# Kernel tuning notes

Hardware: AMD Instinct MI355X
Metric: run time of the kernel (lower is better)

## Reference

```python
import jax, jax.numpy as jnp
import numpy as np

B, S, D, H = 4, 2048, 1024, 16
DH = D // H


def _rope_tables():
    # standard RoPE angle tables, shaped [1, S, 1, DH] as the module expects
    inv_freq = 1.0 / (10000.0 ** (np.arange(0, DH, 2, dtype=np.float32) / DH))
    ang = np.arange(S, dtype=np.float32)[:, None] * inv_freq[None, :]  # [S, DH/2]
    ang = np.concatenate([ang, ang], axis=-1)  # [S, DH]
    cos = jnp.asarray(np.cos(ang))[None, :, None, :]
    sin = jnp.asarray(np.sin(ang))[None, :, None, :]
    return cos, sin


def setup_inputs() -> dict:
    key = jax.random.key(0)
    ks = jax.random.split(key, 5)
    x = jax.random.normal(ks[0], (B, S, D), dtype=jnp.float32)
    wq = jax.random.normal(ks[1], (D, D), dtype=jnp.float32) * 0.02
    wk = jax.random.normal(ks[2], (D, D), dtype=jnp.float32) * 0.02
    wv = jax.random.normal(ks[3], (D, D), dtype=jnp.float32) * 0.02
    wo = jax.random.normal(ks[4], (D, D), dtype=jnp.float32) * 0.02
    cos, sin = _rope_tables()
    return {"x": x, "cos": cos, "sin": sin, "wq": wq, "wk": wk, "wv": wv, "wo": wo}


def _rotate_half(t):
    t1, t2 = t[..., : DH // 2], t[..., DH // 2:]
    return jnp.concatenate([-t2, t1], axis=-1)


def reference(x, cos, sin, wq, wk, wv, wo):
    b, s, d = x.shape
    # QKV projections (torch Linear: y = x @ W.T), reshape to [B, H, S, DH]
    q = (x @ wq.T).reshape(b, s, H, DH).transpose(0, 2, 1, 3)
    k = (x @ wk.T).reshape(b, s, H, DH).transpose(0, 2, 1, 3)
    v = (x @ wv.T).reshape(b, s, H, DH).transpose(0, 2, 1, 3)
    # permute(0,2,1,3): [1,S,1,DH] -> [1,1,S,DH]; slice [:, :s] is a no-op on the size-1 head dim
    cos_p = jnp.transpose(cos, (0, 2, 1, 3))[:, :s]
    sin_p = jnp.transpose(sin, (0, 2, 1, 3))[:, :s]
    q = q * cos_p + _rotate_half(q) * sin_p
    k = k * cos_p + _rotate_half(k) * sin_p
    # SDPA (no mask, dropout_p = 0)
    scores = jnp.einsum("bhqd,bhkd->bhqk", q, k) / jnp.sqrt(jnp.float32(DH))
    attn = jax.nn.softmax(scores, axis=-1)
    out = jnp.einsum("bhqk,bhkd->bhqd", attn, v)
    out = out.transpose(0, 2, 1, 3).reshape(b, s, d)
    return out @ wo.T
```

## Files before the change

kernel.cpp:

```cpp
#include <hip/hip_runtime.h>
#include <hip/hip_bf16.h>
#include <stdint.h>

#define B 4
#define S 2048
#define D 1024
#define H 16
#define DH 64
#define M_TOT (B*S)
#define BH (B*H)

typedef unsigned short u16;
typedef unsigned int u32;
typedef __attribute__((ext_vector_type(4))) float f32x4;
typedef __attribute__((ext_vector_type(16))) float f32x16;
typedef __attribute__((ext_vector_type(8))) short bf16x8;
typedef __attribute__((ext_vector_type(2))) unsigned int u32x2;

typedef const __attribute__((address_space(1))) unsigned int* gp_t;
typedef __attribute__((address_space(3))) unsigned int* lp_t;

__device__ __forceinline__ void gload_lds16(const void* g, void* l) {
    __builtin_amdgcn_global_load_lds((gp_t)g, (lp_t)l, 16, 0, 0);
}

__device__ __forceinline__ float bf2f(u16 u) {
    u32 t = ((u32)u) << 16;
    float f; __builtin_memcpy(&f, &t, 4); return f;
}
__device__ __forceinline__ u16 f2bf(float f) {
    u32 u; __builtin_memcpy(&u, &f, 4);
    u += 0x7fffu + ((u >> 16) & 1u);
    return (u16)(u >> 16);
}
__device__ __forceinline__ u32 packbf(float lo, float hi_) {
    __hip_bfloat162 h = __float22bfloat162_rn(float2{lo, hi_});
    u32 r; __builtin_memcpy(&r, &h, 4); return r;
}

__device__ __forceinline__ float exp2_fast(float x) { return __builtin_amdgcn_exp2f(x); }

#if __has_builtin(__builtin_amdgcn_permlane32_swap)
__device__ __forceinline__ void plswap(u32& a, u32& bb) {
    u32x2 r = __builtin_amdgcn_permlane32_swap(a, bb, false, false);
    a = r.x; bb = r.y;
}
#else
__device__ __forceinline__ void plswap(u32& a, u32& bb) {
    int hi = (threadIdx.x >> 5) & 1;
    u32 ra = (u32)__shfl_xor((int)a, 32);
    u32 rb = (u32)__shfl_xor((int)bb, 32);
    u32 na = hi ? rb : a;
    u32 nb = hi ? bb : ra;
    a = na; bb = nb;
}
#endif

__global__ __launch_bounds__(256)
void cvt_all_kernel(const float* __restrict__ x,
                    const float* __restrict__ wq, const float* __restrict__ wk,
                    const float* __restrict__ wv, const float* __restrict__ wo,
                    u16* __restrict__ xb, u16* __restrict__ wqb, u16* __restrict__ wkb,
                    u16* __restrict__ wvb, u16* __restrict__ wob)
{
    const size_t MD = (size_t)M_TOT * D;
    const size_t WD = (size_t)D * D;
    size_t i = ((size_t)blockIdx.x * 256 + threadIdx.x) * 8;
    const float* src; u16* dst; size_t off;
    if (i < MD) { src = x; dst = xb; off = i; }
    else {
        size_t j = i - MD;
        int wsel = (int)(j >> 20);
        off = j & (WD - 1);
        if      (wsel == 0) { src = wq; dst = wqb; }
        else if (wsel == 1) { src = wk; dst = wkb; }
        else if (wsel == 2) { src = wv; dst = wvb; }
        else                { src = wo; dst = wob; }
    }
    float4 a = *(const float4*)(src + off);
    float4 b = *(const float4*)(src + off + 4);
    union { u16 u[8]; bf16x8 v; } o;
    o.u[0] = f2bf(a.x); o.u[1] = f2bf(a.y); o.u[2] = f2bf(a.z); o.u[3] = f2bf(a.w);
    o.u[4] = f2bf(b.x); o.u[5] = f2bf(b.y); o.u[6] = f2bf(b.z); o.u[7] = f2bf(b.w);
    *(bf16x8*)(dst + off) = o.v;
}

#define NKT 32

__global__ __launch_bounds__(512)
void gemm256_qkv(const u16* __restrict__ X,
                 const u16* __restrict__ W0, const u16* __restrict__ W1, const u16* __restrict__ W2,
                 u16* __restrict__ Y0, u16* __restrict__ Y1, u16* __restrict__ Y2,
                 const float* __restrict__ cosT, const float* __restrict__ sinT)
{
    __shared__ __align__(16) u16 lds[65536];

    const u16* Wm = (blockIdx.z == 0) ? W0 : (blockIdx.z == 1) ? W1 : W2;
    u16* Y        = (blockIdx.z == 0) ? Y0 : (blockIdx.z == 1) ? Y1 : Y2;

    const int t  = threadIdx.x;
    const int w  = t >> 6, ll = t & 63;
    const int lc = ll & 15, g = ll >> 4;
    const int wr = w >> 2, wc = w & 3;
    const int m0 = blockIdx.x * 256, n0 = blockIdx.y * 256;

    const int srow   = t >> 2;
    const int scolsw = 8 * ((t & 3) ^ ((t >> 3) & 3));

    const u16* Xa = X + (size_t)m0 * D;
    const u16* Wa = Wm + (size_t)n0 * D;

    int offA[8], offB[4];
    #pragma unroll
    for (int i = 0; i < 8; ++i) {
        int row = wr * 128 + i * 16 + lc;
        offA[i] = row * 32 + ((g ^ ((row >> 1) & 3)) << 3);
    }
    #pragma unroll
    for (int j = 0; j < 4; ++j) {
        int row = wc * 64 + j * 16 + lc;
        offB[j] = row * 32 + ((g ^ ((row >> 1) & 3)) << 3);
    }

    f32x4 acc[8][4];
    #pragma unroll
    for (int i = 0; i < 8; ++i)
        #pragma unroll
        for (int j = 0; j < 4; ++j)
            acc[i][j] = (f32x4){0.f, 0.f, 0.f, 0.f};

    #pragma unroll
    for (int kt = 0; kt < 3; ++kt) {
        const u16* xs = Xa + (size_t)srow * D + kt * 32 + scolsw;
        gload_lds16(xs,           &lds[kt * 16384 + w * 512]);
        gload_lds16(xs + 128 * D, &lds[kt * 16384 + 4096 + w * 512]);
        const u16* ws = Wa + (size_t)srow * D + kt * 32 + scolsw;
        gload_lds16(ws,           &lds[kt * 16384 + 8192 + w * 512]);
        gload_lds16(ws + 128 * D, &lds[kt * 16384 + 8192 + 4096 + w * 512]);
    }
    asm volatile("s_waitcnt vmcnt(8)" ::: "memory");
    __builtin_amdgcn_s_barrier();

    auto body = [&](int kt, bool do_stage) {
        const int s = kt & 3;
        const u16* As = &lds[s * 16384];
        const u16* Bs = &lds[s * 16384 + 8192];
        const int kn = kt + 3;
        const int sn = kn & 3;
        if (do_stage) {
            const u16* xs = Xa + (size_t)srow * D + kn * 32 + scolsw;
            gload_lds16(xs,           &lds[sn * 16384 + w * 512]);
            gload_lds16(xs + 128 * D, &lds[sn * 16384 + 4096 + w * 512]);
        }
        bf16x8 bfr[4];
        #pragma unroll
        for (int j = 0; j < 4; ++j)
            bfr[j] = *(const bf16x8*)&Bs[offB[j]];
        bf16x8 afr[4];
        #pragma unroll
        for (int i = 0; i < 4; ++i)
            afr[i] = *(const bf16x8*)&As[offA[i]];
        #pragma unroll
        for (int i = 0; i < 4; ++i)
            #pragma unroll
            for (int j = 0; j < 4; ++j)
                acc[i][j] = __builtin_amdgcn_mfma_f32_16x16x32_bf16(afr[i], bfr[j], acc[i][j], 0, 0, 0);
        if (do_stage) {
            const u16* ws = Wa + (size_t)srow * D + kn * 32 + scolsw;
            gload_lds16(ws,           &lds[sn * 16384 + 8192 + w * 512]);
            gload_lds16(ws + 128 * D, &lds[sn * 16384 + 8192 + 4096 + w * 512]);
        }
        #pragma unroll
        for (int i = 0; i < 4; ++i)
            afr[i] = *(const bf16x8*)&As[offA[i + 4]];
        #pragma unroll
        for (int i = 0; i < 4; ++i)
            #pragma unroll
            for (int j = 0; j < 4; ++j)
                acc[i + 4][j] = __builtin_amdgcn_mfma_f32_16x16x32_bf16(afr[i], bfr[j], acc[i + 4][j], 0, 0, 0);
    };

    for (int kt = 0; kt < NKT - 3; ++kt) {
        body(kt, true);
        asm volatile("s_waitcnt vmcnt(8)" ::: "memory");
        __builtin_amdgcn_s_barrier();
    }
    body(NKT - 3, false);
    asm volatile("s_waitcnt vmcnt(4)" ::: "memory");
    __builtin_amdgcn_s_barrier();
    body(NKT - 2, false);
    asm volatile("s_waitcnt vmcnt(0)" ::: "memory");
    __builtin_amdgcn_s_barrier();
    body(NKT - 1, false);

    if (blockIdx.z < 2) {
        const float scale = (blockIdx.z == 0) ? (0.125f * 1.44269504f) : 1.0f;
        #pragma unroll
        for (int i = 0; i < 8; ++i)
            #pragma unroll
            for (int r = 0; r < 4; ++r) {
                int row = m0 + wr * 128 + i * 16 + g * 4 + r;
                int s = row & (S - 1);
                #pragma unroll
                for (int jh = 0; jh < 2; ++jh) {
                    float c  = cosT[s * DH + jh * 16 + lc];
                    float sn = sinT[s * DH + jh * 16 + lc];
                    float a0 = acc[i][jh][r], a1 = acc[i][jh + 2][r];
                    size_t base = (size_t)row * D + n0 + wc * 64;
                    Y[base + jh * 16 + lc]       = f2bf((a0 * c - a1 * sn) * scale);
                    Y[base + (jh + 2) * 16 + lc] = f2bf((a1 * c + a0 * sn) * scale);
                }
            }
    } else {
        #pragma unroll
        for (int i = 0; i < 8; ++i)
            #pragma unroll
            for (int j = 0; j < 4; ++j) {
                int row = m0 + wr * 128 + i * 16 + g * 4;
                int col = n0 + wc * 64 + j * 16 + lc;
                int bt = row >> 11, s = row & (S - 1);
                size_t vtrow = (size_t)(bt * 16 + (col >> 6)) * 64 + (col & 63);
                u32 w0 = packbf(acc[i][j][0], acc[i][j][1]);
                u32 w1 = packbf(acc[i][j][2], acc[i][j][3]);
                u32x2 pr; pr.x = w0; pr.y = w1;
                *(u32x2*)&Y[vtrow * S + s] = pr;
            }
    }
}

__global__ __launch_bounds__(256)
void gemm128_wo(const u16* __restrict__ X, const u16* __restrict__ Wm,
                float* __restrict__ Y)
{
    __shared__ __align__(16) u16 lds[32768];

    const int t  = threadIdx.x;
    const int w  = t >> 6, ll = t & 63;
    const int lc = ll & 15, g = ll >> 4;
    const int wr = w >> 1, wc = w & 1;
    const int m0 = blockIdx.x * 128, n0 = blockIdx.y * 128;

    const int srow   = t >> 2;
    const int scolsw = 8 * ((t & 3) ^ ((t >> 3) & 3));

    const u16* Xa = X + (size_t)m0 * D;
    const u16* Wa = Wm + (size_t)n0 * D;

    int offA[4], offB[4];
    #pragma unroll
    for (int i = 0; i < 4; ++i) {
        int row = wr * 64 + i * 16 + lc;
        offA[i] = row * 32 + ((g ^ ((row >> 1) & 3)) << 3);
    }
    #pragma unroll
    for (int j = 0; j < 4; ++j) {
        int row = wc * 64 + j * 16 + lc;
        offB[j] = row * 32 + ((g ^ ((row >> 1) & 3)) << 3);
    }

    f32x4 acc[4][4];
    #pragma unroll
    for (int i = 0; i < 4; ++i)
        #pragma unroll
        for (int j = 0; j < 4; ++j)
            acc[i][j] = (f32x4){0.f, 0.f, 0.f, 0.f};

    #pragma unroll
    for (int kt = 0; kt < 3; ++kt) {
        const u16* xs = Xa + (size_t)srow * D + kt * 32 + scolsw;
        gload_lds16(xs,          &lds[kt * 8192 + w * 512]);
        gload_lds16(xs + 64 * D, &lds[kt * 8192 + 2048 + w * 512]);
        const u16* ws = Wa + (size_t)srow * D + kt * 32 + scolsw;
        gload_lds16(ws,          &lds[kt * 8192 + 4096 + w * 512]);
        gload_lds16(ws + 64 * D, &lds[kt * 8192 + 4096 + 2048 + w * 512]);
    }
    asm volatile("s_waitcnt vmcnt(8)" ::: "memory");
    __builtin_amdgcn_s_barrier();

    auto body = [&](int kt, bool do_stage) {
        const int s = kt & 3;
        const u16* As = &lds[s * 8192];
        const u16* Bs = &lds[s * 8192 + 4096];
        const int kn = kt + 3;
        const int sn = kn & 3;
        if (do_stage) {
            const u16* xs = Xa + (size_t)srow * D + kn * 32 + scolsw;
            gload_lds16(xs,          &lds[sn * 8192 + w * 512]);
            gload_lds16(xs + 64 * D, &lds[sn * 8192 + 2048 + w * 512]);
        }
        bf16x8 bfr[4];
        #pragma unroll
        for (int j = 0; j < 4; ++j)
            bfr[j] = *(const bf16x8*)&Bs[offB[j]];
        bf16x8 afr[2];
        afr[0] = *(const bf16x8*)&As[offA[0]];
        afr[1] = *(const bf16x8*)&As[offA[1]];
        #pragma unroll
        for (int i = 0; i < 2; ++i)
            #pragma unroll
            for (int j = 0; j < 4; ++j)
                acc[i][j] = __builtin_amdgcn_mfma_f32_16x16x32_bf16(afr[i], bfr[j], acc[i][j], 0, 0, 0);
        if (do_stage) {
            const u16* ws = Wa + (size_t)srow * D + kn * 32 + scolsw;
            gload_lds16(ws,          &lds[sn * 8192 + 4096 + w * 512]);
            gload_lds16(ws + 64 * D, &lds[sn * 8192 + 4096 + 2048 + w * 512]);
        }
        afr[0] = *(const bf16x8*)&As[offA[2]];
        afr[1] = *(const bf16x8*)&As[offA[3]];
        #pragma unroll
        for (int i = 0; i < 2; ++i)
            #pragma unroll
            for (int j = 0; j < 4; ++j)
                acc[i + 2][j] = __builtin_amdgcn_mfma_f32_16x16x32_bf16(afr[i], bfr[j], acc[i + 2][j], 0, 0, 0);
    };

    for (int kt = 0; kt < NKT - 3; ++kt) {
        body(kt, true);
        asm volatile("s_waitcnt vmcnt(8)" ::: "memory");
        __builtin_amdgcn_s_barrier();
    }
    body(NKT - 3, false);
    asm volatile("s_waitcnt vmcnt(4)" ::: "memory");
    __builtin_amdgcn_s_barrier();
    body(NKT - 2, false);
    asm volatile("s_waitcnt vmcnt(0)" ::: "memory");
    __builtin_amdgcn_s_barrier();
    body(NKT - 1, false);

    #pragma unroll
    for (int i = 0; i < 4; ++i)
        #pragma unroll
        for (int j = 0; j < 4; ++j)
            #pragma unroll
            for (int r = 0; r < 4; ++r) {
                int row = m0 + wr * 64 + i * 16 + g * 4 + r;
                int col = n0 + wc * 64 + j * 16 + lc;
                Y[(size_t)row * D + col] = acc[i][j][r];
            }
}

#define QBLK 256
#define KVT 128
#define NT (S / KVT)

__global__ __launch_bounds__(256, 2)
void attn_mfma(const u16* __restrict__ Q, const u16* __restrict__ Kg,
               const u16* __restrict__ Vt, u16* __restrict__ CTX)
{
    __shared__ __align__(16) u16 smem[32768];

    const int t  = threadIdx.x;
    const int w  = t >> 6;
    const int q  = t & 31;
    const int hi = (t >> 5) & 1;

    const int bid  = blockIdx.x;
    const int xcd  = bid & 7;
    const int slot = bid >> 3;
    const int bh   = xcd * 8 + (slot >> 3);
    const int qb   = slot & 7;
    const int b = bh >> 4, h = bh & 15;
    const int q0 = qb * QBLK;
    const int qbase = q0 + w * 64;

    bf16x8 qf[2][4];
    #pragma unroll
    for (int qg = 0; qg < 2; ++qg) {
        const u16* qp = &Q[(size_t)(b*S + qbase + qg*32 + q) * D + h*DH + hi*8];
        qf[qg][0] = *(const bf16x8*)(qp);
        qf[qg][1] = *(const bf16x8*)(qp + 16);
        qf[qg][2] = *(const bf16x8*)(qp + 32);
        qf[qg][3] = *(const bf16x8*)(qp + 48);
    }

    bf16x8 ones;
    {
        union { u16 u[8]; bf16x8 v; } ou;
        #pragma unroll
        for (int i = 0; i < 8; ++i) ou.u[i] = 0x3f80;
        ones = ou.v;
    }

    f32x16 po[4], lsum[2], zv;
    #pragma unroll
    for (int i = 0; i < 16; ++i) {
        po[0][i] = 0.f; po[1][i] = 0.f; po[2][i] = 0.f; po[3][i] = 0.f;
        lsum[0][i] = 0.f; lsum[1][i] = 0.f; zv[i] = 0.f;
    }

    const int ksrow = t >> 3;
    const int kscol = (((t & 7) << 4) ^ ((ksrow & 7) << 4)) >> 1;
    const int vsrow = t >> 4;
    const int vscol = (((t & 15) ^ (vsrow & 15)) << 3);
    const int rsw  = (q & 7) << 4;
    const int vsw  = (q & 15) << 4;

    u16* buf0 = smem;
    u16* buf1 = smem + 16384;

    const u16* kg = Kg + ((size_t)(b * S) + ksrow) * D + (size_t)h * DH + kscol;
    const u16* vg = Vt + ((size_t)bh * DH + vsrow) * S + vscol;

    #define STAGE(dst) do {                                         \
        gload_lds16(kg,           (dst) + 0*2048 + w*512);          \
        gload_lds16(kg + 32*D,    (dst) + 1*2048 + w*512);          \
        gload_lds16(kg + 64*D,    (dst) + 2*2048 + w*512);          \
        gload_lds16(kg + 96*D,    (dst) + 3*2048 + w*512);          \
        gload_lds16(vg,           (dst) + 8192 + 0*2048 + w*512);   \
        gload_lds16(vg + 16*S,    (dst) + 8192 + 1*2048 + w*512);   \
        gload_lds16(vg + 32*S,    (dst) + 8192 + 2*2048 + w*512);   \
        gload_lds16(vg + 48*S,    (dst) + 8192 + 3*2048 + w*512);   \
        kg += (size_t)KVT * D; vg += KVT; } while (0)

    auto compute = [&](const u16* base) {
        const u16* Kl = base;
        const u16* Vl = base + 8192;
        #pragma unroll
        for (int c = 0; c < 4; ++c) {
            f32x16 p0, p1;
            {
                const u16* kr = &Kl[(c*32 + q) << 6];
                bf16x8 k0 = *(const bf16x8*)&kr[((0*32 + hi*16) ^ rsw) >> 1];
                __builtin_amdgcn_s_setprio(1);
                p0 = __builtin_amdgcn_mfma_f32_32x32x16_bf16(k0, qf[0][0], zv, 0, 0, 0);
                p1 = __builtin_amdgcn_mfma_f32_32x32x16_bf16(k0, qf[1][0], zv, 0, 0, 0);
                #pragma unroll
                for (int cc = 1; cc < 4; ++cc) {
                    bf16x8 kf = *(const bf16x8*)&kr[((cc*32 + hi*16) ^ rsw) >> 1];
                    p0 = __builtin_amdgcn_mfma_f32_32x32x16_bf16(kf, qf[0][cc], p0, 0, 0, 0);
                    p1 = __builtin_amdgcn_mfma_f32_32x32x16_bf16(kf, qf[1][cc], p1, 0, 0, 0);
                }
                __builtin_amdgcn_s_setprio(0);
            }

            u32 W0[8], W1[8];
            #pragma unroll
            for (int j = 0; j < 8; ++j) {
                W0[j] = packbf(exp2_fast(p0[2*j]), exp2_fast(p0[2*j + 1]));
                W1[j] = packbf(exp2_fast(p1[2*j]), exp2_fast(p1[2*j + 1]));
            }
            plswap(W0[0], W0[2]); plswap(W0[1], W0[3]);
            plswap(W0[4], W0[6]); plswap(W0[5], W0[7]);
            plswap(W1[0], W1[2]); plswap(W1[1], W1[3]);
            plswap(W1[4], W1[6]); plswap(W1[5], W1[7]);
            bf16x8 pa0a, pa0b, pa1a, pa1b;
            {
                union { u32 u[4]; bf16x8 v; } pb;
                pb.u[0]=W0[0]; pb.u[1]=W0[1]; pb.u[2]=W0[2]; pb.u[3]=W0[3]; pa0a = pb.v;
                pb.u[0]=W0[4]; pb.u[1]=W0[5]; pb.u[2]=W0[6]; pb.u[3]=W0[7]; pa0b = pb.v;
                pb.u[0]=W1[0]; pb.u[1]=W1[1]; pb.u[2]=W1[2]; pb.u[3]=W1[3]; pa1a = pb.v;
                pb.u[0]=W1[4]; pb.u[1]=W1[5]; pb.u[2]=W1[6]; pb.u[3]=W1[7]; pa1b = pb.v;
            }

            __builtin_amdgcn_s_setprio(1);
            lsum[0] = __builtin_amdgcn_mfma_f32_32x32x16_bf16(ones, pa0a, lsum[0], 0, 0, 0);
            lsum[1] = __builtin_amdgcn_mfma_f32_32x32x16_bf16(ones, pa1a, lsum[1], 0, 0, 0);
            lsum[0] = __builtin_amdgcn_mfma_f32_32x32x16_bf16(ones, pa0b, lsum[0], 0, 0, 0);
            lsum[1] = __builtin_amdgcn_mfma_f32_32x32x16_bf16(ones, pa1b, lsum[1], 0, 0, 0);
            #pragma unroll
            for (int kk = 0; kk < 2; ++kk) {
                int vb = ((c*64 + kk*32 + hi*16) ^ vsw) >> 1;
                bf16x8 v0 = *(const bf16x8*)&Vl[(q << 7) + vb];
                bf16x8 v1 = *(const bf16x8*)&Vl[((32 + q) << 7) + vb];
                bf16x8 pq0 = kk ? pa0b : pa0a;
                bf16x8 pq1 = kk ? pa1b : pa1a;
                po[0] = __builtin_amdgcn_mfma_f32_32x32x16_bf16(v0, pq0, po[0], 0, 0, 0);
                po[1] = __builtin_amdgcn_mfma_f32_32x32x16_bf16(v1, pq0, po[1], 0, 0, 0);
                po[2] = __builtin_amdgcn_mfma_f32_32x32x16_bf16(v0, pq1, po[2], 0, 0, 0);
                po[3] = __builtin_amdgcn_mfma_f32_32x32x16_bf16(v1, pq1, po[3], 0, 0, 0);
            }
            __builtin_amdgcn_s_setprio(0);
        }
    };

    STAGE(buf0);
    asm volatile("s_waitcnt vmcnt(0)" ::: "memory");
    __builtin_amdgcn_s_barrier();

    for (int ti = 0; ti < NT; ti += 2) {
        STAGE(buf1);
        compute(buf0);
        asm volatile("s_waitcnt vmcnt(0)" ::: "memory");
        __builtin_amdgcn_s_barrier();
        if (ti < NT - 2) STAGE(buf0);
        compute(buf1);
        asm volatile("s_waitcnt vmcnt(0)" ::: "memory");
        __builtin_amdgcn_s_barrier();
    }
    #undef STAGE

    u16* ow = &smem[w * 2304];
    #pragma unroll
    for (int qg = 0; qg < 2; ++qg) {
        float inv = 1.f / lsum[qg][0];
        #pragma unroll
        for (int r = 0; r < 16; ++r) {
            int d0 = (r & 3) + 8 * (r >> 2) + 4 * hi;
            ow[q * 72 + d0]      = f2bf(po[qg*2 + 0][r] * inv);
            ow[q * 72 + 32 + d0] = f2bf(po[qg*2 + 1][r] * inv);
        }
        int row = (t & 63) >> 1, half = t & 1;
        const u16* orow = &ow[row * 72 + half * 32];
        u16* gp = &CTX[(size_t)(b*S + qbase + qg*32 + row) * D + h*DH + half * 32];
        #pragma unroll
        for (int i = 0; i < 4; ++i)
            *(bf16x8*)(gp + i * 8) = *(const bf16x8*)(orow + i * 8);
    }
}

extern "C" void kernel_launch(void* const* d_in, const int* in_sizes, int n_in,
                              void* d_out, int out_size, void* d_ws, size_t ws_size,
                              hipStream_t stream)
{
    const float* x    = (const float*)d_in[0];
    const float* cosT = (const float*)d_in[1];
    const float* sinT = (const float*)d_in[2];
    const float* wq   = (const float*)d_in[3];
    const float* wk   = (const float*)d_in[4];
    const float* wv   = (const float*)d_in[5];
    const float* wo   = (const float*)d_in[6];
    float* out = (float*)d_out;

    const size_t MD = (size_t)M_TOT * D;
    const size_t WD = (size_t)D * D;

    u16* xb   = (u16*)d_ws;
    u16* Qb   = xb + MD;
    u16* Kb   = Qb + MD;
    u16* Vtb  = Kb + MD;
    u16* CTXb = Vtb + MD;
    u16* wqb  = CTXb + MD;
    u16* wkb  = wqb + WD;
    u16* wvb  = wkb + WD;
    u16* wob  = wvb + WD;

    cvt_all_kernel<<<(int)((MD + 4*WD) / 8 / 256), 256, 0, stream>>>(
        x, wq, wk, wv, wo, xb, wqb, wkb, wvb, wob);

    gemm256_qkv<<<dim3(M_TOT / 256, D / 256, 3), 512, 0, stream>>>(
        xb, wqb, wkb, wvb, Qb, Kb, Vtb, cosT, sinT);

    attn_mfma<<<dim3(M_TOT / QBLK * H), 256, 0, stream>>>(Qb, Kb, Vtb, CTXb);

    gemm128_wo<<<dim3(M_TOT / 128, D / 128), 256, 0, stream>>>(
        CTXb, wob, out);
}
```

Measured before the change: 177.4 us.

## Use four-stage KV pipeline with 64-key tiles in attention kernel

Replaces the double-buffered 128-key K/V staging in the attention kernel with a four-slot ring of 64-key tiles that prefetches three tiles ahead. Waits use partial vmcnt so loads stay in flight across iterations instead of draining to zero each step. The V tile layout and swizzle change to match the 64-wide rows. This adds more barriers per key and smaller tiles, which may raise synchronisation overhead.

```diff
diff --git a/kernel.cpp b/kernel.cpp
--- a/kernel.cpp
+++ b/kernel.cpp
@@ -340,8 +340,8 @@
 }
 
 #define QBLK 256
-#define KVT 128
-#define NT (S / KVT)
+#define KVT2 64
+#define NTT (S / KVT2)
 
 __global__ __launch_bounds__(256, 2)
 void attn_mfma(const u16* __restrict__ Q, const u16* __restrict__ Kg,
@@ -388,35 +388,27 @@
         lsum[0][i] = 0.f; lsum[1][i] = 0.f; zv[i] = 0.f;
     }
 
-    const int ksrow = t >> 3;
-    const int kscol = (((t & 7) << 4) ^ ((ksrow & 7) << 4)) >> 1;
-    const int vsrow = t >> 4;
-    const int vscol = (((t & 15) ^ (vsrow & 15)) << 3);
+    const int srow = t >> 3;
+    const int scol = ((t & 7) ^ ((t >> 3) & 7)) << 3;
     const int rsw  = (q & 7) << 4;
-    const int vsw  = (q & 15) << 4;
-
-    u16* buf0 = smem;
-    u16* buf1 = smem + 16384;
-
-    const u16* kg = Kg + ((size_t)(b * S) + ksrow) * D + (size_t)h * DH + kscol;
-    const u16* vg = Vt + ((size_t)bh * DH + vsrow) * S + vscol;
-
-    #define STAGE(dst) do {                                         \
-        gload_lds16(kg,           (dst) + 0*2048 + w*512);          \
-        gload_lds16(kg + 32*D,    (dst) + 1*2048 + w*512);          \
-        gload_lds16(kg + 64*D,    (dst) + 2*2048 + w*512);          \
-        gload_lds16(kg + 96*D,    (dst) + 3*2048 + w*512);          \
-        gload_lds16(vg,           (dst) + 8192 + 0*2048 + w*512);   \
-        gload_lds16(vg + 16*S,    (dst) + 8192 + 1*2048 + w*512);   \
-        gload_lds16(vg + 32*S,    (dst) + 8192 + 2*2048 + w*512);   \
-        gload_lds16(vg + 48*S,    (dst) + 8192 + 3*2048 + w*512);   \
-        kg += (size_t)KVT * D; vg += KVT; } while (0)
-
-    auto compute = [&](const u16* base) {
-        const u16* Kl = base;
-        const u16* Vl = base + 8192;
-        #pragma unroll
-        for (int c = 0; c < 4; ++c) {
+
+    const u16* kg = Kg + ((size_t)(b * S) + srow) * D + (size_t)h * DH + scol;
+    const u16* vg = Vt + ((size_t)bh * DH + srow) * S + scol;
+
+    #define STAGE(sl) do {                                       \
+        gload_lds16(kg,          &smem[(sl)*8192 + w*512]);          \
+        gload_lds16(kg + 32*D,   &smem[(sl)*8192 + 2048 + w*512]);   \
+        gload_lds16(vg,          &smem[(sl)*8192 + 4096 + w*512]);   \
+        gload_lds16(vg + 32*S,   &smem[(sl)*8192 + 4096 + 2048 + w*512]); \
+        kg += (size_t)KVT2 * D; vg += KVT2; } while (0)
+
+    auto body = [&](int kt, bool do_stage) {
+        const int sl = kt & 3;
+        const u16* Kl = &smem[sl * 8192];
+        const u16* Vl = &smem[sl * 8192 + 4096];
+        if (do_stage) { const int sn = (kt + 3) & 3; STAGE(sn); }
+        #pragma unroll
+        for (int c = 0; c < 2; ++c) {
             f32x16 p0, p1;
             {
                 const u16* kr = &Kl[(c*32 + q) << 6];
@@ -459,9 +451,9 @@
             lsum[1] = __builtin_amdgcn_mfma_f32_32x32x16_bf16(ones, pa1b, lsum[1], 0, 0, 0);
             #pragma unroll
             for (int kk = 0; kk < 2; ++kk) {
-                int vb = ((c*64 + kk*32 + hi*16) ^ vsw) >> 1;
-                bf16x8 v0 = *(const bf16x8*)&Vl[(q << 7) + vb];
-                bf16x8 v1 = *(const bf16x8*)&Vl[((32 + q) << 7) + vb];
+                int vb = ((c*64 + kk*32 + hi*16) ^ rsw) >> 1;
+                bf16x8 v0 = *(const bf16x8*)&Vl[(q << 6) + vb];
+                bf16x8 v1 = *(const bf16x8*)&Vl[((32 + q) << 6) + vb];
                 bf16x8 pq0 = kk ? pa0b : pa0a;
                 bf16x8 pq1 = kk ? pa1b : pa1a;
                 po[0] = __builtin_amdgcn_mfma_f32_32x32x16_bf16(v0, pq0, po[0], 0, 0, 0);
@@ -473,20 +465,22 @@
         }
     };
 
-    STAGE(buf0);
+    STAGE(0); STAGE(1); STAGE(2);
+    asm volatile("s_waitcnt vmcnt(8)" ::: "memory");
+    __builtin_amdgcn_s_barrier();
+
+    for (int kt = 0; kt < NTT - 3; ++kt) {
+        body(kt, true);
+        asm volatile("s_waitcnt vmcnt(8)" ::: "memory");
+        __builtin_amdgcn_s_barrier();
+    }
+    body(NTT - 3, false);
+    asm volatile("s_waitcnt vmcnt(4)" ::: "memory");
+    __builtin_amdgcn_s_barrier();
+    body(NTT - 2, false);
     asm volatile("s_waitcnt vmcnt(0)" ::: "memory");
     __builtin_amdgcn_s_barrier();
-
-    for (int ti = 0; ti < NT; ti += 2) {
-        STAGE(buf1);
-        compute(buf0);
-        asm volatile("s_waitcnt vmcnt(0)" ::: "memory");
-        __builtin_amdgcn_s_barrier();
-        if (ti < NT - 2) STAGE(buf0);
-        compute(buf1);
-        asm volatile("s_waitcnt vmcnt(0)" ::: "memory");
-        __builtin_amdgcn_s_barrier();
-    }
+    body(NTT - 1, false);
     #undef STAGE
 
     u16* ow = &smem[w * 2304];
```

Result: no change. 178.2 us (+0.5%).
